# Optimization experiments

Measured on AMD Instinct MI355X. Metric: run time of the kernel, lower is better.

The kernel has to match this reference:

```python
import jax, jax.numpy as jnp
import numpy as np

H = 512          # hidden_size of the active GRU_with_GCC
IN = 2048        # input_size of stream 1 (the encoded stream)
FS = 1536        # feats_size of stream 0 (auxiliary GCC stream)
B, T = 128, 64


def setup_inputs() -> dict:
    key = jax.random.key(0)
    ks = jax.random.split(key, 8)
    stdv = 1.0 / np.sqrt(H)
    u = lambda k, shape: jax.random.uniform(k, shape, jnp.float32, -stdv, stdv)
    return {
        "feat0": jax.random.normal(ks[0], (B, T, FS), jnp.float32),
        "feat1": jax.random.normal(ks[1], (B, T, IN), jnp.float32),
        "W_ih": u(ks[2], (3 * H, IN)),
        "b_ih": u(ks[3], (3 * H,)),
        "W_hh": u(ks[4], (3 * H, H)),
        "b_hh": u(ks[5], (3 * H,)),
        "W_fh": u(ks[6], (2 * H, FS)),
        "b_fh": u(ks[7], (2 * H,)),
    }


def reference(feat0, feat1, W_ih, b_ih, W_hh, b_hh, W_fh, b_fh):
    # Encoder_Baseline (eval mode -> dropout is identity), skip_info=[1,0]:
    # only stream 1 is encoded by GRU_with_GCC with feat0 as auxiliary gating.
    # Precompute input and auxiliary projections for all timesteps (batched GEMM).
    gi = jnp.einsum('bti,gi->btg', feat1, W_ih) + b_ih   # [B,T,3H]
    gf = jnp.einsum('btf,gf->btg', feat0, W_fh) + b_fh   # [B,T,2H]

    def step(h, inp):
        gi_t, gf_t = inp                                  # [B,3H], [B,2H]
        gh = h @ W_hh.T + b_hh                            # [B,3H]
        i_r, i_i, i_n = jnp.split(gi_t, 3, axis=-1)
        h_r, h_i, h_n = jnp.split(gh, 3, axis=-1)
        f_r, f_i = jnp.split(gf_t, 2, axis=-1)
        resetgate = jax.nn.sigmoid(i_r + h_r + f_r)
        inputgate = jax.nn.sigmoid(i_i + h_i + f_i)
        newgate = jnp.tanh(i_n + resetgate * h_n)
        hy = newgate + inputgate * (h - newgate)
        return hy, hy

    h0 = jnp.zeros((feat1.shape[0], H), feat1.dtype)
    hT, ys = jax.lax.scan(step, h0, (gi.transpose(1, 0, 2), gf.transpose(1, 0, 2)))
    eo = ys.transpose(1, 0, 2)                            # [B,T,H]
    return eo, hT
```

## Files before the change

### kernel.cpp

```cpp
#include <hip/hip_runtime.h>
#include <cstdint>
#include <cstddef>

typedef __bf16 bf16_t;
typedef bf16_t bf16x8 __attribute__((ext_vector_type(8)));
typedef float floatx4 __attribute__((ext_vector_type(4)));
typedef unsigned long long u64;

#define B_   128
#define T_   64
#define H_   512
#define IN_  2048
#define FS_  1536
#define M_   (B_ * T_)
#define GB_  64
#define SENT (~0ull)

__device__ __forceinline__ void async16(void* lds, const void* gp) {
  __builtin_amdgcn_global_load_lds(
      (const __attribute__((address_space(1))) void*)gp,
      (__attribute__((address_space(3))) void*)lds, 16, 0, 0);
}

__device__ __forceinline__ u64 cload64(const u64* p) {
  return __hip_atomic_load((u64*)p, __ATOMIC_RELAXED, __HIP_MEMORY_SCOPE_AGENT);
}
__device__ __forceinline__ void cstore64(u64* p, u64 v) {
  __hip_atomic_store(p, v, __ATOMIC_RELAXED, __HIP_MEMORY_SCOPE_AGENT);
}

__device__ __forceinline__ float fsigmoid(float x) {
  return __builtin_amdgcn_rcpf(1.f + __expf(-x));
}
__device__ __forceinline__ float ftanh(float x) {
  return 2.f * __builtin_amdgcn_rcpf(1.f + __expf(-2.f * x)) - 1.f;
}

__global__ __launch_bounds__(256) void cvt_bf16_k(const float* __restrict__ s,
                                                  bf16_t* __restrict__ d, int n8) {
  int i = blockIdx.x * 256 + threadIdx.x;
  if (i >= n8) return;
  const float4* s4 = (const float4*)s;
  float4 v0 = s4[2 * (size_t)i];
  float4 v1 = s4[2 * (size_t)i + 1];
  bf16x8 o;
  o[0] = (bf16_t)v0.x; o[1] = (bf16_t)v0.y; o[2] = (bf16_t)v0.z; o[3] = (bf16_t)v0.w;
  o[4] = (bf16_t)v1.x; o[5] = (bf16_t)v1.y; o[6] = (bf16_t)v1.z; o[7] = (bf16_t)v1.w;
  *(bf16x8*)(d + (size_t)i * 8) = o;
}

#define BM 128
#define BN 128
#define BK 32

__global__ __launch_bounds__(256) void gemm_bt_bias(
    const bf16_t* __restrict__ A, const bf16_t* __restrict__ B,
    const float* __restrict__ bias, float* __restrict__ C,
    int M, int N, int K) {
  __shared__ __align__(16) bf16_t As[BM * BK];
  __shared__ __align__(16) bf16_t Bs[BN * BK];

  const int tid  = threadIdx.x;
  const int lane = tid & 63;
  const int wave = tid >> 6;
  const int wr = wave >> 1, wc = wave & 1;
  const int mblk = blockIdx.y * BM;
  const int nblk = blockIdx.x * BN;

  const int sr = lane >> 2;
  const int sc = (lane & 3) * 8;
  const int c0 = wave * 2;

  const bf16_t* Ag0 = A + (size_t)(mblk + c0 * 16 + sr) * K + sc;
  const bf16_t* Ag1 = A + (size_t)(mblk + c0 * 16 + 16 + sr) * K + sc;
  const bf16_t* Bg0 = B + (size_t)(nblk + c0 * 16 + sr) * K + sc;
  const bf16_t* Bg1 = B + (size_t)(nblk + c0 * 16 + 16 + sr) * K + sc;
  bf16_t* As0 = As + c0 * 512;
  bf16_t* Bs0 = Bs + c0 * 512;

  floatx4 acc[4][4] = {};

  const int fm = lane & 15;
  const int fk = (lane >> 4) * 8;

  for (int kt = 0; kt < K; kt += BK) {
    async16(As0,       Ag0 + kt);
    async16(As0 + 512, Ag1 + kt);
    async16(Bs0,       Bg0 + kt);
    async16(Bs0 + 512, Bg1 + kt);
    __syncthreads();

    bf16x8 a[4], b[4];
#pragma unroll
    for (int i = 0; i < 4; i++)
      a[i] = *(const bf16x8*)(As + (wr * 64 + i * 16 + fm) * BK + fk);
#pragma unroll
    for (int j = 0; j < 4; j++)
      b[j] = *(const bf16x8*)(Bs + (wc * 64 + j * 16 + fm) * BK + fk);
#pragma unroll
    for (int i = 0; i < 4; i++)
#pragma unroll
      for (int j = 0; j < 4; j++)
        acc[i][j] = __builtin_amdgcn_mfma_f32_16x16x32_bf16(a[i], b[j], acc[i][j], 0, 0, 0);
    __syncthreads();
  }

  const int en  = nblk + wc * 64 + (lane & 15);
  const int em0 = mblk + wr * 64 + (lane >> 4) * 4;
#pragma unroll
  for (int j = 0; j < 4; j++) {
    int col = en + j * 16;
    float bv = bias[col];
#pragma unroll
    for (int i = 0; i < 4; i++) {
#pragma unroll
      for (int r = 0; r < 4; r++) {
        int row = em0 + i * 16 + r;
        C[(size_t)row * N + col] = acc[i][j][r] + bv;
      }
    }
  }
}

__global__ __launch_bounds__(256) void gru_scan(
    const float* __restrict__ Whh_f,
    const float* __restrict__ bhh,
    const float* __restrict__ gi,
    const float* __restrict__ gf,
    bf16_t* __restrict__ hbuf,
    float* __restrict__ out) {
  __shared__ __align__(16) bf16_t wlds[48 * 64 * 8];
  __shared__ __align__(16) bf16_t swp[4][256];

  const int tid  = threadIdx.x;
  const int lane = tid & 63;
  const int w    = tid >> 6;
  const int lm   = lane & 15;
  const int lq   = lane >> 4;
  const int c    = blockIdx.x >> 1;
  const int mh   = blockIdx.x & 1;
  const int n0   = c * 16;

  for (int f = w; f < 48; f += 4) {
    int g = f >> 4, kt = f & 15;
    const float* src = Whh_f + (size_t)(g * H_ + n0 + lm) * H_ + kt * 32 + lq * 8;
    float4 v0 = *(const float4*)src;
    float4 v1 = *(const float4*)(src + 4);
    bf16x8 o;
    o[0] = (bf16_t)v0.x; o[1] = (bf16_t)v0.y; o[2] = (bf16_t)v0.z; o[3] = (bf16_t)v0.w;
    o[4] = (bf16_t)v1.x; o[5] = (bf16_t)v1.y; o[6] = (bf16_t)v1.z; o[7] = (bf16_t)v1.w;
    *(bf16x8*)(wlds + (f * 64 + lane) * 8) = o;
  }

  {
    u64* z = (u64*)(hbuf + (((size_t)mh * 32 + c) * 64 + w * 16) * 16) + lane;
    cstore64(z, 0ull);
  }
  __syncthreads();

  const float b0 = bhh[n0 + lm];
  const float b1 = bhh[H_ + n0 + lm];
  const float b2 = bhh[2 * H_ + n0 + lm];

  const int m0 = mh * 64 + w * 16;
  float hp[4] = {0.f, 0.f, 0.f, 0.f};

  float pir[4], pii[4], pin[4], pfr[4], pfi[4];
  auto prefetch = [&](int t) {
#pragma unroll
    for (int r = 0; r < 4; ++r) {
      size_t mrow = (size_t)(m0 + lq * 4 + r) * T_ + t;
      const float* gip = gi + mrow * (3 * H_) + n0 + lm;
      pir[r] = gip[0];
      pii[r] = gip[H_];
      pin[r] = gip[2 * H_];
      const float* gfp = gf + mrow * (2 * H_) + n0 + lm;
      pfr[r] = gfp[0];
      pfi[r] = gfp[H_];
    }
  };
  prefetch(0);

  const size_t habase = (size_t)mh * 32768 + ((size_t)w * 16 + lm) * 16 +
                        (size_t)(lq >> 1) * 1024 + (lq & 1) * 8;

  for (int t = 0; t < T_; ++t) {
    const bf16_t* hstep = hbuf + (size_t)t * 65536;
    union { u64 u[2]; bf16x8 v; } a[16];
    for (;;) {
      int ok = 1;
#pragma unroll
      for (int kt = 0; kt < 16; ++kt) {
        const u64* ap = (const u64*)(hstep + habase + (size_t)kt * 2048);
        a[kt].u[0] = cload64(ap);
        a[kt].u[1] = cload64(ap + 1);
      }
#pragma unroll
      for (int kt = 0; kt < 16; ++kt)
        ok &= (a[kt].u[0] != SENT) & (a[kt].u[1] != SENT);
      if (__all(ok)) break;
      __builtin_amdgcn_s_sleep(1);
    }

    floatx4 acc[3] = {};
#pragma unroll
    for (int g = 0; g < 3; ++g)
#pragma unroll
      for (int kt = 0; kt < 16; ++kt) {
        bf16x8 b = *(const bf16x8*)(wlds + ((g * 16 + kt) * 64 + lane) * 8);
        acc[g] = __builtin_amdgcn_mfma_f32_16x16x32_bf16(a[kt].v, b, acc[g], 0, 0, 0);
      }

    float hy[4];
#pragma unroll
    for (int r = 0; r < 4; ++r) {
      float rg = fsigmoid(pir[r] + acc[0][r] + b0 + pfr[r]);
      float ig = fsigmoid(pii[r] + acc[1][r] + b1 + pfi[r]);
      float ng = ftanh(pin[r] + rg * (acc[2][r] + b2));
      hy[r] = ng + ig * (hp[r] - ng);
      hp[r] = hy[r];
      swp[w][(lq * 4 + r) * 16 + lm] = (bf16_t)hy[r];
    }

    if (t + 1 < T_) {
      asm volatile("s_waitcnt lgkmcnt(0)" ::: "memory");
      u64 pk = *(const u64*)(&swp[w][0] + lane * 4);
      u64* dst = (u64*)(hbuf + (size_t)(t + 1) * 65536 +
                        (((size_t)mh * 32 + c) * 64 + w * 16) * 16) + lane;
      cstore64(dst, pk);
    }

#pragma unroll
    for (int r = 0; r < 4; ++r) {
      int brow = m0 + lq * 4 + r;
      size_t mrow = (size_t)brow * T_ + t;
      out[mrow * H_ + n0 + lm] = hy[r];
      if (t == T_ - 1)
        out[(size_t)M_ * H_ + (size_t)brow * H_ + n0 + lm] = hy[r];
    }
    if (t + 1 < T_) prefetch(t + 1);
  }
}

extern "C" void kernel_launch(void* const* d_in, const int* in_sizes, int n_in,
                              void* d_out, int out_size, void* d_ws, size_t ws_size,
                              hipStream_t stream) {
  const float* feat0 = (const float*)d_in[0];
  const float* feat1 = (const float*)d_in[1];
  const float* W_ih  = (const float*)d_in[2];
  const float* b_ih  = (const float*)d_in[3];
  const float* W_hh  = (const float*)d_in[4];
  const float* b_hh  = (const float*)d_in[5];
  const float* W_fh  = (const float*)d_in[6];
  const float* b_fh  = (const float*)d_in[7];
  float* out = (float*)d_out;

  char* p = (char*)d_ws;
  float*  gi   = (float*)p;  p += (size_t)M_ * 3 * H_ * 4;
  float*  gf   = (float*)p;  p += (size_t)M_ * 2 * H_ * 4;
  bf16_t* A1   = (bf16_t*)p; p += (size_t)M_ * IN_ * 2;
  bf16_t* A0   = (bf16_t*)p; p += (size_t)M_ * FS_ * 2;
  bf16_t* Wihb = (bf16_t*)p; p += (size_t)3 * H_ * IN_ * 2;
  bf16_t* Wfhb = (bf16_t*)p; p += (size_t)2 * H_ * FS_ * 2;

  bf16_t* hbuf = A0;

  auto cvt = [&](const float* s, bf16_t* d, size_t n) {
    int n8 = (int)(n / 8);
    cvt_bf16_k<<<(n8 + 255) / 256, 256, 0, stream>>>(s, d, n8);
  };
  cvt(feat1, A1, (size_t)M_ * IN_);
  cvt(feat0, A0, (size_t)M_ * FS_);
  cvt(W_ih, Wihb, (size_t)3 * H_ * IN_);
  cvt(W_fh, Wfhb, (size_t)2 * H_ * FS_);

  gemm_bt_bias<<<dim3((3 * H_) / BN, M_ / BM), 256, 0, stream>>>(
      A1, Wihb, b_ih, gi, M_, 3 * H_, IN_);
  gemm_bt_bias<<<dim3((2 * H_) / BN, M_ / BM), 256, 0, stream>>>(
      A0, Wfhb, b_fh, gf, M_, 2 * H_, FS_);

  hipMemsetAsync(hbuf, 0xFF, (size_t)T_ * 65536 * sizeof(bf16_t), stream);

  gru_scan<<<GB_, 256, 0, stream>>>(W_hh, b_hh, gi, gf, hbuf, out);
}
```

Before: 521.5 us.

## Fuse projection GEMMs and GRU scan into one producer-consumer persistent kernel

Merges the two input-projection GEMMs and the recurrent scan into a single launch. 64 blocks run the GRU scan while 384 producer blocks compute per-timestep GEMM tiles and signal per-timestep counters, so the scan can start before all projections are finished. Inputs are transposed to time-major during bf16 conversion so each job covers one timestep, and the gf projection is stored as fp16 to cut traffic. The risks are spin-wait overhead, producers competing with scan blocks for CUs, and the precision loss from fp16 gf.

```diff
diff --git a/kernel.cpp b/kernel.cpp
--- a/kernel.cpp
+++ b/kernel.cpp
@@ -14,7 +14,13 @@
 #define FS_  1536
 #define M_   (B_ * T_)
 #define GB_  64
+#define PROD_ 384
+#define JOBS_ 1280
 #define SENT (~0ull)
+
+#define BM 128
+#define BN 128
+#define BK 32
 
 __device__ __forceinline__ void async16(void* lds, const void* gp) {
   __builtin_amdgcn_global_load_lds(
@@ -26,6 +32,15 @@
   return __hip_atomic_load((u64*)p, __ATOMIC_RELAXED, __HIP_MEMORY_SCOPE_AGENT);
 }
 __device__ __forceinline__ void cstore64(u64* p, u64 v) {
+  __hip_atomic_store(p, v, __ATOMIC_RELAXED, __HIP_MEMORY_SCOPE_AGENT);
+}
+__device__ __forceinline__ int cloadi(const int* p) {
+  return __hip_atomic_load((int*)p, __ATOMIC_RELAXED, __HIP_MEMORY_SCOPE_AGENT);
+}
+__device__ __forceinline__ void cstoref(float* p, float v) {
+  __hip_atomic_store(p, v, __ATOMIC_RELAXED, __HIP_MEMORY_SCOPE_AGENT);
+}
+__device__ __forceinline__ void cstoreh(unsigned short* p, unsigned short v) {
   __hip_atomic_store(p, v, __ATOMIC_RELAXED, __HIP_MEMORY_SCOPE_AGENT);
 }
 
@@ -49,97 +64,135 @@
   *(bf16x8*)(d + (size_t)i * 8) = o;
 }
 
-#define BM 128
-#define BN 128
-#define BK 32
-
-__global__ __launch_bounds__(256) void gemm_bt_bias(
-    const bf16_t* __restrict__ A, const bf16_t* __restrict__ B,
-    const float* __restrict__ bias, float* __restrict__ C,
-    int M, int N, int K) {
-  __shared__ __align__(16) bf16_t As[BM * BK];
-  __shared__ __align__(16) bf16_t Bs[BN * BK];
-
-  const int tid  = threadIdx.x;
-  const int lane = tid & 63;
-  const int wave = tid >> 6;
-  const int wr = wave >> 1, wc = wave & 1;
-  const int mblk = blockIdx.y * BM;
-  const int nblk = blockIdx.x * BN;
-
-  const int sr = lane >> 2;
-  const int sc = (lane & 3) * 8;
-  const int c0 = wave * 2;
-
-  const bf16_t* Ag0 = A + (size_t)(mblk + c0 * 16 + sr) * K + sc;
-  const bf16_t* Ag1 = A + (size_t)(mblk + c0 * 16 + 16 + sr) * K + sc;
-  const bf16_t* Bg0 = B + (size_t)(nblk + c0 * 16 + sr) * K + sc;
-  const bf16_t* Bg1 = B + (size_t)(nblk + c0 * 16 + 16 + sr) * K + sc;
-  bf16_t* As0 = As + c0 * 512;
-  bf16_t* Bs0 = Bs + c0 * 512;
-
-  floatx4 acc[4][4] = {};
-
-  const int fm = lane & 15;
-  const int fk = (lane >> 4) * 8;
-
-  for (int kt = 0; kt < K; kt += BK) {
-    async16(As0,       Ag0 + kt);
-    async16(As0 + 512, Ag1 + kt);
-    async16(Bs0,       Bg0 + kt);
-    async16(Bs0 + 512, Bg1 + kt);
-    __syncthreads();
-
-    bf16x8 a[4], b[4];
-#pragma unroll
-    for (int i = 0; i < 4; i++)
-      a[i] = *(const bf16x8*)(As + (wr * 64 + i * 16 + fm) * BK + fk);
-#pragma unroll
-    for (int j = 0; j < 4; j++)
-      b[j] = *(const bf16x8*)(Bs + (wc * 64 + j * 16 + fm) * BK + fk);
-#pragma unroll
-    for (int i = 0; i < 4; i++)
-#pragma unroll
-      for (int j = 0; j < 4; j++)
-        acc[i][j] = __builtin_amdgcn_mfma_f32_16x16x32_bf16(a[i], b[j], acc[i][j], 0, 0, 0);
-    __syncthreads();
-  }
-
-  const int en  = nblk + wc * 64 + (lane & 15);
-  const int em0 = mblk + wr * 64 + (lane >> 4) * 4;
-#pragma unroll
-  for (int j = 0; j < 4; j++) {
-    int col = en + j * 16;
-    float bv = bias[col];
-#pragma unroll
-    for (int i = 0; i < 4; i++) {
-#pragma unroll
-      for (int r = 0; r < 4; r++) {
-        int row = em0 + i * 16 + r;
-        C[(size_t)row * N + col] = acc[i][j][r] + bv;
-      }
-    }
-  }
-}
-
-__global__ __launch_bounds__(256) void gru_scan(
-    const float* __restrict__ Whh_f,
-    const float* __restrict__ bhh,
-    const float* __restrict__ gi,
-    const float* __restrict__ gf,
+__global__ __launch_bounds__(256) void cvt_t_k(const float* __restrict__ s,
+                                               bf16_t* __restrict__ d,
+                                               int Kv, int n8) {
+  int g = blockIdx.x * 256 + threadIdx.x;
+  if (g >= n8) return;
+  int kg = Kv >> 3;
+  int k8 = g % kg;
+  int row = g / kg;
+  int b = row >> 6, t = row & 63;
+  const float4* s4 = (const float4*)(s + (size_t)row * Kv + k8 * 8);
+  float4 v0 = s4[0], v1 = s4[1];
+  bf16x8 o;
+  o[0] = (bf16_t)v0.x; o[1] = (bf16_t)v0.y; o[2] = (bf16_t)v0.z; o[3] = (bf16_t)v0.w;
+  o[4] = (bf16_t)v1.x; o[5] = (bf16_t)v1.y; o[6] = (bf16_t)v1.z; o[7] = (bf16_t)v1.w;
+  *(bf16x8*)(d + (size_t)(t * 128 + b) * Kv + k8 * 8) = o;
+}
+
+__global__ __launch_bounds__(256) void uber(
+    const bf16_t* __restrict__ A1t, const bf16_t* __restrict__ A0t,
+    const bf16_t* __restrict__ Wihb, const bf16_t* __restrict__ Wfhb,
+    const float* __restrict__ b_ih, const float* __restrict__ b_fh,
+    const float* __restrict__ Whh_f, const float* __restrict__ bhh,
+    float* __restrict__ gi,
+    _Float16* __restrict__ gfh,
     bf16_t* __restrict__ hbuf,
+    int* __restrict__ cnt,
     float* __restrict__ out) {
-  __shared__ __align__(16) bf16_t wlds[48 * 64 * 8];
-  __shared__ __align__(16) bf16_t swp[4][256];
-
+  __shared__ __align__(16) char smem[51200];
   const int tid  = threadIdx.x;
   const int lane = tid & 63;
   const int w    = tid >> 6;
-  const int lm   = lane & 15;
-  const int lq   = lane >> 4;
-  const int c    = blockIdx.x >> 1;
-  const int mh   = blockIdx.x & 1;
-  const int n0   = c * 16;
+
+  if (blockIdx.x >= GB_) {
+    bf16_t* As = (bf16_t*)smem;
+    bf16_t* Bs = (bf16_t*)(smem + 8192);
+    const int wr = w >> 1, wc = w & 1;
+    const int sr = lane >> 2;
+    const int sc = (lane & 3) * 8;
+    const int c0 = w * 2;
+    const int fm = lane & 15;
+    const int fk = (lane >> 4) * 8;
+    const int pid = blockIdx.x - GB_;
+
+    for (int job = pid; job < JOBS_; job += PROD_) {
+      const int t = job / 20, sub = job % 20;
+      const bool g1 = sub < 12;
+      const int K = g1 ? IN_ : FS_;
+      const int N = g1 ? 1536 : 1024;
+      const int nblk = (g1 ? sub : sub - 12) * BN;
+      const bf16_t* A  = (g1 ? A1t : A0t) + (size_t)t * 128 * K;
+      const bf16_t* Bw = g1 ? Wihb : Wfhb;
+      const float* bias = g1 ? b_ih : b_fh;
+
+      const bf16_t* Ag0 = A + (size_t)(c0 * 16 + sr) * K + sc;
+      const bf16_t* Ag1 = A + (size_t)(c0 * 16 + 16 + sr) * K + sc;
+      const bf16_t* Bg0 = Bw + (size_t)(nblk + c0 * 16 + sr) * K + sc;
+      const bf16_t* Bg1 = Bw + (size_t)(nblk + c0 * 16 + 16 + sr) * K + sc;
+      bf16_t* As0 = As + c0 * 512;
+      bf16_t* Bs0 = Bs + c0 * 512;
+
+      floatx4 acc[4][4] = {};
+      for (int kt = 0; kt < K; kt += BK) {
+        async16(As0,       Ag0 + kt);
+        async16(As0 + 512, Ag1 + kt);
+        async16(Bs0,       Bg0 + kt);
+        async16(Bs0 + 512, Bg1 + kt);
+        __syncthreads();
+        bf16x8 a[4], b[4];
+#pragma unroll
+        for (int i = 0; i < 4; i++)
+          a[i] = *(const bf16x8*)(As + (wr * 64 + i * 16 + fm) * BK + fk);
+#pragma unroll
+        for (int j = 0; j < 4; j++)
+          b[j] = *(const bf16x8*)(Bs + (wc * 64 + j * 16 + fm) * BK + fk);
+#pragma unroll
+        for (int i = 0; i < 4; i++)
+#pragma unroll
+          for (int j = 0; j < 4; j++)
+            acc[i][j] = __builtin_amdgcn_mfma_f32_16x16x32_bf16(a[i], b[j], acc[i][j], 0, 0, 0);
+        __syncthreads();
+      }
+
+      const int en  = nblk + wc * 64 + fm;
+      const int em0 = wr * 64 + (lane >> 4) * 4;
+      if (g1) {
+        float* C = gi + (size_t)t * 128 * 1536;
+#pragma unroll
+        for (int j = 0; j < 4; j++) {
+          int col = en + j * 16;
+          float bv = bias[col];
+#pragma unroll
+          for (int i = 0; i < 4; i++)
+#pragma unroll
+            for (int r = 0; r < 4; r++)
+              cstoref(&C[(size_t)(em0 + i * 16 + r) * 1536 + col], acc[i][j][r] + bv);
+        }
+      } else {
+        _Float16* C = gfh + (size_t)t * 128 * 1024;
+#pragma unroll
+        for (int j = 0; j < 4; j++) {
+          int col = en + j * 16;
+          float bv = bias[col];
+#pragma unroll
+          for (int i = 0; i < 4; i++)
+#pragma unroll
+            for (int r = 0; r < 4; r++) {
+              _Float16 hv = (_Float16)(acc[i][j][r] + bv);
+              cstoreh((unsigned short*)&C[(size_t)(em0 + i * 16 + r) * 1024 + col],
+                      __builtin_bit_cast(unsigned short, hv));
+            }
+        }
+      }
+      asm volatile("s_waitcnt vmcnt(0)" ::: "memory");
+      __syncthreads();
+      if (tid == 0)
+        __hip_atomic_fetch_add(cnt + t, 1, __ATOMIC_RELAXED, __HIP_MEMORY_SCOPE_AGENT);
+    }
+    return;
+  }
+
+  asm volatile("s_setprio 3" ::: );
+  bf16_t* wlds = (bf16_t*)smem;
+  bf16_t* swp  = (bf16_t*)(smem + 49152);
+
+  const int lm = lane & 15;
+  const int lq = lane >> 4;
+  const int c  = blockIdx.x >> 1;
+  const int mh = blockIdx.x & 1;
+  const int n0 = c * 16;
 
   for (int f = w; f < 48; f += 4) {
     int g = f >> 4, kt = f & 15;
@@ -167,16 +220,17 @@
 
   float pir[4], pii[4], pin[4], pfr[4], pfi[4];
   auto prefetch = [&](int t) {
+    while (cloadi(cnt + t) < 20) __builtin_amdgcn_s_sleep(1);
 #pragma unroll
     for (int r = 0; r < 4; ++r) {
-      size_t mrow = (size_t)(m0 + lq * 4 + r) * T_ + t;
-      const float* gip = gi + mrow * (3 * H_) + n0 + lm;
-      pir[r] = gip[0];
-      pii[r] = gip[H_];
-      pin[r] = gip[2 * H_];
-      const float* gfp = gf + mrow * (2 * H_) + n0 + lm;
-      pfr[r] = gfp[0];
-      pfi[r] = gfp[H_];
+      int brow = m0 + lq * 4 + r;
+      const float* gp = gi + ((size_t)t * 128 + brow) * 1536 + n0 + lm;
+      pir[r] = gp[0];
+      pii[r] = gp[512];
+      pin[r] = gp[1024];
+      const _Float16* fp = gfh + ((size_t)t * 128 + brow) * 1024 + n0 + lm;
+      pfr[r] = (float)fp[0];
+      pfi[r] = (float)fp[512];
     }
   };
   prefetch(0);
@@ -219,12 +273,12 @@
       float ng = ftanh(pin[r] + rg * (acc[2][r] + b2));
       hy[r] = ng + ig * (hp[r] - ng);
       hp[r] = hy[r];
-      swp[w][(lq * 4 + r) * 16 + lm] = (bf16_t)hy[r];
+      swp[w * 256 + (lq * 4 + r) * 16 + lm] = (bf16_t)hy[r];
     }
 
     if (t + 1 < T_) {
       asm volatile("s_waitcnt lgkmcnt(0)" ::: "memory");
-      u64 pk = *(const u64*)(&swp[w][0] + lane * 4);
+      u64 pk = *(const u64*)(swp + w * 256 + lane * 4);
       u64* dst = (u64*)(hbuf + (size_t)(t + 1) * 65536 +
                         (((size_t)mh * 32 + c) * 64 + w * 16) * 16) + lane;
       cstore64(dst, pk);
@@ -256,30 +310,35 @@
   float* out = (float*)d_out;
 
   char* p = (char*)d_ws;
-  float*  gi   = (float*)p;  p += (size_t)M_ * 3 * H_ * 4;
-  float*  gf   = (float*)p;  p += (size_t)M_ * 2 * H_ * 4;
-  bf16_t* A1   = (bf16_t*)p; p += (size_t)M_ * IN_ * 2;
-  bf16_t* A0   = (bf16_t*)p; p += (size_t)M_ * FS_ * 2;
-  bf16_t* Wihb = (bf16_t*)p; p += (size_t)3 * H_ * IN_ * 2;
-  bf16_t* Wfhb = (bf16_t*)p; p += (size_t)2 * H_ * FS_ * 2;
-
-  bf16_t* hbuf = A0;
-
-  auto cvt = [&](const float* s, bf16_t* d, size_t n) {
-    int n8 = (int)(n / 8);
-    cvt_bf16_k<<<(n8 + 255) / 256, 256, 0, stream>>>(s, d, n8);
-  };
-  cvt(feat1, A1, (size_t)M_ * IN_);
-  cvt(feat0, A0, (size_t)M_ * FS_);
-  cvt(W_ih, Wihb, (size_t)3 * H_ * IN_);
-  cvt(W_fh, Wfhb, (size_t)2 * H_ * FS_);
-
-  gemm_bt_bias<<<dim3((3 * H_) / BN, M_ / BM), 256, 0, stream>>>(
-      A1, Wihb, b_ih, gi, M_, 3 * H_, IN_);
-  gemm_bt_bias<<<dim3((2 * H_) / BN, M_ / BM), 256, 0, stream>>>(
-      A0, Wfhb, b_fh, gf, M_, 2 * H_, FS_);
-
-  hipMemsetAsync(hbuf, 0xFF, (size_t)T_ * 65536 * sizeof(bf16_t), stream);
-
-  gru_scan<<<GB_, 256, 0, stream>>>(W_hh, b_hh, gi, gf, hbuf, out);
-}
+  int*      cnt  = (int*)p;      p += 4096;
+  bf16_t*   hbuf = (bf16_t*)p;   p += (size_t)T_ * 65536 * 2;
+  float*    gi   = (float*)p;    p += (size_t)M_ * 3 * H_ * 4;
+  _Float16* gfh  = (_Float16*)p; p += (size_t)M_ * 2 * H_ * 2;
+  bf16_t*   A1t  = (bf16_t*)p;   p += (size_t)M_ * IN_ * 2;
+  bf16_t*   A0t  = (bf16_t*)p;   p += (size_t)M_ * FS_ * 2;
+  bf16_t*   Wihb = (bf16_t*)p;   p += (size_t)3 * H_ * IN_ * 2;
+  bf16_t*   Wfhb = (bf16_t*)p;   p += (size_t)2 * H_ * FS_ * 2;
+
+  hipMemsetAsync(cnt, 0, 4096, stream);
+  hipMemsetAsync(hbuf, 0xFF, (size_t)T_ * 65536 * 2, stream);
+
+  {
+    int n8 = M_ * IN_ / 8;
+    cvt_t_k<<<(n8 + 255) / 256, 256, 0, stream>>>(feat1, A1t, IN_, n8);
+  }
+  {
+    int n8 = M_ * FS_ / 8;
+    cvt_t_k<<<(n8 + 255) / 256, 256, 0, stream>>>(feat0, A0t, FS_, n8);
+  }
+  {
+    int n8 = 3 * H_ * IN_ / 8;
+    cvt_bf16_k<<<(n8 + 255) / 256, 256, 0, stream>>>(W_ih, Wihb, n8);
+  }
+  {
+    int n8 = 2 * H_ * FS_ / 8;
+    cvt_bf16_k<<<(n8 + 255) / 256, 256, 0, stream>>>(W_fh, Wfhb, n8);
+  }
+
+  uber<<<GB_ + PROD_, 256, 0, stream>>>(A1t, A0t, Wihb, Wfhb, b_ih, b_fh,
+                                        W_hh, b_hh, gi, gfh, hbuf, cnt, out);
+}
```

New measurement: 592.1 us. 1.14x slower.
